# Optimization experiments

Measured on AMD Instinct MI355X. Metric: run time of the kernel, lower is better.

The kernel has to match this reference:

```python
import jax, jax.numpy as jnp
import numpy as np

BLOCK = 4  # block_size from init_kwargs


def space_to_channel_3d(x, b):
    # Faithful translation of SpaceToChannel_3d.forward (torch split/stack/permute chain).
    B, C, W, H, D = x.shape
    y = x.transpose(0, 2, 3, 4, 1)                      # (B, W, H, D, C)
    y = y.reshape(B, W, H, D // b, b, C)                # split depth into D//b chunks of b
    y = y.transpose(0, 3, 1, 2, 4, 5)                   # (B, D//b, W, H, b, C)
    y = y.reshape(B, D // b, W // b, H // b, C * b * b * b)  # per-chunk row-major reshape
    y = y.transpose(0, 2, 3, 1, 4)                      # (B, W//b, H//b, D//b, C*b^3)
    return y.transpose(0, 4, 1, 2, 3)                   # (B, C*b^3, W//b, H//b, D//b)


def channel_to_space_3d(x, b):
    # Faithful translation of ChannelToSpace_3d.forward.
    B, Cd, wd, hd, dd = x.shape
    b3 = b * b * b
    Cs = Cd // b3
    y = x.transpose(0, 2, 3, 4, 1)                      # (B, wd, hd, dd, Cd)
    y = y.reshape(B, wd, hd, dd, b * b, b, Cs)          # split b^3 dim into b^2 chunks of b
    y = y.transpose(0, 4, 1, 2, 3, 5, 6)                # (B, b^2, wd, hd, dd, b, Cs)
    y = y.reshape(B, b * b, wd, hd, dd * b, Cs)         # merge (dd, b) per chunk
    y = y.transpose(0, 2, 1, 3, 4, 5)                   # (B, wd, b^2, hd, dd*b, Cs)
    y = y.reshape(B, wd * b, hd * b, dd * b, Cs)        # row-major merge of (wd, b^2, hd)
    return y.transpose(0, 4, 1, 2, 3)                   # (B, Cs, wd*b, hd*b, dd*b)


def setup_inputs() -> dict:
    key = jax.random.key(0)
    k1, k2 = jax.random.split(key)
    x = jax.random.normal(k1, (4, 32, 64, 64, 64), dtype=jnp.float32)
    gamma = jax.random.normal(k2, (1,), dtype=jnp.float32)
    return {"x": x, "gamma": gamma}


def reference(x, gamma):
    b = BLOCK
    y = space_to_channel_3d(x, b)                       # (B, C*b^3, w, h, d)
    B, C, w, h, d = y.shape
    q = y.reshape(B, C, w * h * d)                      # (B, C', N)
    # channel-wise attention: energy (B, C', C')
    energy = jnp.einsum('bcn,ben->bce', q, q)
    energy_new = jnp.max(energy, axis=-1, keepdims=True) - energy
    attention = jax.nn.softmax(energy_new, axis=-1)
    out = jnp.einsum('bce,ben->bcn', attention, q)      # (B, C', N)
    out = out.reshape(B, C, w, h, d)
    out = gamma * out + y
    return channel_to_space_3d(out, b)
```

## Files before the change

### kernel.cpp

```cpp
#include <hip/hip_runtime.h>

typedef _Float16 f16;
typedef __attribute__((ext_vector_type(8))) _Float16 f16x8;
typedef __attribute__((ext_vector_type(4))) float f32x4;

#define CCH 2048
#define NSP 4096
#define NB  4

#define VMCNT8 asm volatile("s_waitcnt vmcnt(8)" ::: "memory")
#define VMCNT4 asm volatile("s_waitcnt vmcnt(4)" ::: "memory")
#define VMCNT0 asm volatile("s_waitcnt vmcnt(0)" ::: "memory")
#define CFENCE asm volatile("" ::: "memory")

__device__ __forceinline__ void gld16(const void* g, void* l) {
  __builtin_amdgcn_global_load_lds(
      (const __attribute__((address_space(1))) void*)g,
      (__attribute__((address_space(3))) void*)l, 16, 0, 0);
}

__global__ void pack_kernel(const float* __restrict__ x, f16* __restrict__ qh,
                            f16* __restrict__ qv, int b0) {
  int gid = blockIdx.x * 256 + threadIdx.x;
  int n = gid & (NSP - 1);
  int t = gid >> 12;
  int c = t & 31; t >>= 5;
  int r = t & 15; int ib = t >> 4;
  int wc = n >> 8, hc = (n >> 4) & 15, dc = n & 15;
  int w = wc * 4 + (hc >> 2);
  int h = (hc & 3) * 16 + r;
  int b = b0 + ib;
  const f32x4 v = *(const f32x4*)(x + ((((size_t)b * 32 + c) * 64 + w) * 64 + h) * 64 + dc * 4);
#pragma unroll
  for (int bd = 0; bd < 4; ++bd) {
    int cc = r * 128 + bd * 32 + c;
    size_t o = ((size_t)ib * CCH + cc) * NSP + n;
    float val = v[bd];
    f16 hi = (f16)val;
    qh[o] = hi;
    qv[o] = (f16)(2.0f * val - (float)hi);
  }
}

__global__ void transpose_kernel(const f16* __restrict__ qh, f16* __restrict__ qhT) {
  int ib = blockIdx.z;
  int j0 = blockIdx.x * 64, n0 = blockIdx.y * 64;
  __shared__ f16 tile[64][72];
  int t = threadIdx.x;
  int r = t >> 3;
  int cb = (t & 7) * 8;
#pragma unroll
  for (int half = 0; half < 2; ++half) {
    int rr = r + half * 32;
    f16x8 v = *(const f16x8*)(qh + ((size_t)ib * CCH + j0 + rr) * NSP + n0 + cb);
    *(f16x8*)&tile[rr][cb] = v;
  }
  __syncthreads();
#pragma unroll
  for (int half = 0; half < 2; ++half) {
    int rr = r + half * 32;
    f16x8 o;
#pragma unroll
    for (int u = 0; u < 8; ++u) o[u] = tile[cb + u][rr];
    *(f16x8*)(qhT + ((size_t)ib * NSP + n0 + rr) * CCH + j0 + cb) = o;
  }
}

__global__ __launch_bounds__(256) void gemm1_kernel(const f16* __restrict__ qh,
                                                    const f16* __restrict__ qv,
                                                    float* __restrict__ energy) {
  int ib = blockIdx.z;
  int bx = blockIdx.x;
  int tri = (bx & 7) * 17 + (bx >> 3);
  int rem = tri, bi = 0, span = 16;
  while (rem >= span) { rem -= span; ++bi; --span; }
  int bj = bi + rem;
  int i0 = bi * 128, j0 = bj * 128;
  float* eout = energy + (size_t)ib * CCH * CCH;

  __shared__ f16 Lds[2][4][128 * 32];
  int tid = threadIdx.x;
  int lane = tid & 63, wv = tid >> 6;
  int l15 = lane & 15, quad = lane >> 4;
  int wr = (wv >> 1) * 64, wcol = (wv & 1) * 64;
  int swz = (l15 >> 1) & 3;
  int kbs = (lane & 3) ^ ((lane >> 3) & 3);

  const f16* srcA = (wv & 1) ? qv : qh;
  int rbase = (wv < 2) ? i0 : j0;
  const f16* gsrc = srcA + ((size_t)ib * CCH + rbase) * NSP
                    + (size_t)(lane >> 2) * NSP + kbs * 8;

  auto stage = [&](int buf, int kk) {
    f16* ld = &Lds[buf][wv][0];
#pragma unroll
    for (int t = 0; t < 8; ++t)
      gld16(gsrc + (size_t)(t * 16) * NSP + kk, ld + t * 512);
  };

  const f32x4 vzero = {0.f, 0.f, 0.f, 0.f};
  f32x4 acc[4][4];
#pragma unroll
  for (int a = 0; a < 4; ++a)
#pragma unroll
    for (int bq = 0; bq < 4; ++bq) acc[a][bq] = vzero;

  const int nk = NSP >> 5;
  stage(0, 0);
  __syncthreads();
  for (int it = 0; it < nk; ++it) {
    int cur = it & 1;
    if (it + 1 < nk) stage(cur ^ 1, (it + 1) << 5);
    f16x8 ah[4], av[4], bh[4], bv[4];
#pragma unroll
    for (int mt = 0; mt < 4; ++mt) {
      int row = wr + mt * 16 + l15;
      ah[mt] = *(const f16x8*)&Lds[cur][0][row * 32 + ((quad ^ swz) * 8)];
      av[mt] = *(const f16x8*)&Lds[cur][1][row * 32 + ((quad ^ swz) * 8)];
    }
#pragma unroll
    for (int nt = 0; nt < 4; ++nt) {
      int col = wcol + nt * 16 + l15;
      bh[nt] = *(const f16x8*)&Lds[cur][2][col * 32 + ((quad ^ swz) * 8)];
      bv[nt] = *(const f16x8*)&Lds[cur][3][col * 32 + ((quad ^ swz) * 8)];
    }
    __builtin_amdgcn_s_setprio(1);
#pragma unroll
    for (int mt = 0; mt < 4; ++mt)
#pragma unroll
      for (int nt = 0; nt < 4; ++nt) {
        acc[mt][nt] = __builtin_amdgcn_mfma_f32_16x16x32_f16(ah[mt], bv[nt], acc[mt][nt], 0, 0, 0);
        acc[mt][nt] = __builtin_amdgcn_mfma_f32_16x16x32_f16(av[mt], bh[nt], acc[mt][nt], 0, 0, 0);
      }
    __builtin_amdgcn_s_setprio(0);
    __syncthreads();
  }
  bool diag = (bi == bj);
#pragma unroll
  for (int mt = 0; mt < 4; ++mt)
#pragma unroll
    for (int nt = 0; nt < 4; ++nt)
#pragma unroll
      for (int rg = 0; rg < 4; ++rg) {
        int row = i0 + wr + mt * 16 + quad * 4 + rg;
        int col = j0 + wcol + nt * 16 + l15;
        float v = 0.5f * acc[mt][nt][rg];
        eout[(size_t)row * CCH + col] = v;
        if (!diag) eout[(size_t)col * CCH + row] = v;
      }
}

__global__ void softmax_kernel(const float* __restrict__ e0,
                               const float* __restrict__ gamma_p,
                               f16* __restrict__ attn) {
  int i = blockIdx.x, ib = blockIdx.y;
  const float* r0 = e0 + ((size_t)ib * CCH + i) * CCH;
  f16* arow = attn + ((size_t)ib * CCH + i) * CCH;
  int t = threadIdx.x;
  f32x4 v0 = *(const f32x4*)(r0 + t * 8);
  f32x4 v1 = *(const f32x4*)(r0 + t * 8 + 4);
  float m = v0[0];
#pragma unroll
  for (int u = 1; u < 4; ++u) m = fminf(m, v0[u]);
#pragma unroll
  for (int u = 0; u < 4; ++u) m = fminf(m, v1[u]);
#pragma unroll
  for (int off = 32; off > 0; off >>= 1) m = fminf(m, __shfl_xor(m, off));
  __shared__ float redA[4], redB[4];
  if ((t & 63) == 0) redA[t >> 6] = m;
  __syncthreads();
  m = fminf(fminf(redA[0], redA[1]), fminf(redA[2], redA[3]));
  float e[8], s = 0.f;
#pragma unroll
  for (int u = 0; u < 4; ++u) { e[u] = __expf(m - v0[u]); s += e[u]; }
#pragma unroll
  for (int u = 0; u < 4; ++u) { e[4 + u] = __expf(m - v1[u]); s += e[4 + u]; }
#pragma unroll
  for (int off = 32; off > 0; off >>= 1) s += __shfl_xor(s, off);
  if ((t & 63) == 0) redB[t >> 6] = s;
  __syncthreads();
  s = redB[0] + redB[1] + redB[2] + redB[3];
  float gamma = *gamma_p;
  float ginv = gamma / s;
  int du = i - t * 8;
  f16x8 o;
#pragma unroll
  for (int u = 0; u < 8; ++u) {
    float v = e[u] * ginv;
    if (u == du) v += 1.0f;
    o[u] = (f16)v;
  }
  *(f16x8*)(arow + t * 8) = o;
}

__global__ __launch_bounds__(256) void gemm2_kernel(const f16* __restrict__ attn,
                                                    const f16* __restrict__ qhT,
                                                    float* __restrict__ out, int b0) {
  int ib = blockIdx.z;
  int lin = blockIdx.x + gridDim.x * blockIdx.y;
  int nwg = gridDim.x * gridDim.y;
  int cpx = nwg >> 3;
  int lin2 = (lin & 7) * cpx + (lin >> 3);
  int i0 = (lin2 & 15) * 128;
  int n0 = (lin2 >> 4) * 128;
  __shared__ f16 Lds[4][2][128 * 32];
  int tid = threadIdx.x;
  int lane = tid & 63, wv = tid >> 6;
  int l15 = lane & 15, quad = lane >> 4;
  int wr = (wv >> 1) * 64, wcol = (wv & 1) * 64;
  int swz = (l15 >> 1) & 3;
  int kbs = (lane & 3) ^ ((lane >> 3) & 3);

  int arr = wv >> 1, rh = wv & 1;
  const f16* gbase = arr ? (qhT + ((size_t)ib * NSP + n0) * CCH)
                         : (attn + ((size_t)ib * CCH + i0) * CCH);
  const f16* gsrc = gbase + (size_t)(rh * 64 + (lane >> 2)) * CCH + kbs * 8;

  auto stage = [&](int slot, int kk) {
#pragma unroll
    for (int t = 0; t < 4; ++t)
      gld16(gsrc + (size_t)(t * 16) * CCH + kk,
            &Lds[slot][arr][(rh * 64 + t * 16) * 32]);
  };

  const f32x4 vzero = {0.f, 0.f, 0.f, 0.f};
  f32x4 acc[4][4];
#pragma unroll
  for (int a = 0; a < 4; ++a)
#pragma unroll
    for (int bq = 0; bq < 4; ++bq) acc[a][bq] = vzero;

  const int NP = CCH / 32;
  stage(0, 0); stage(1, 32); stage(2, 64);
  for (int p = 0; p < NP; ++p) {
    int remp = NP - 1 - p;
    if (remp >= 2) { VMCNT8; } else if (remp == 1) { VMCNT4; } else { VMCNT0; }
    __builtin_amdgcn_s_barrier();
    CFENCE;
    if (p + 3 < NP) stage((p + 3) & 3, (p + 3) << 5);
    int s = p & 3;
    const f16* As = &Lds[s][0][0];
    const f16* Bs = &Lds[s][1][0];
    f16x8 af[4], bf[4];
#pragma unroll
    for (int mt = 0; mt < 4; ++mt)
      af[mt] = *(const f16x8*)&As[(wr + mt * 16 + l15) * 32 + ((quad ^ swz) * 8)];
#pragma unroll
    for (int nt = 0; nt < 4; ++nt)
      bf[nt] = *(const f16x8*)&Bs[(wcol + nt * 16 + l15) * 32 + ((quad ^ swz) * 8)];
    __builtin_amdgcn_s_setprio(1);
#pragma unroll
    for (int mt = 0; mt < 4; ++mt)
#pragma unroll
      for (int nt = 0; nt < 4; ++nt)
        acc[mt][nt] = __builtin_amdgcn_mfma_f32_16x16x32_f16(af[mt], bf[nt], acc[mt][nt], 0, 0, 0);
    __builtin_amdgcn_s_setprio(0);
  }

  __syncthreads();
  float* eld = (float*)&Lds[0][0][0];
#pragma unroll
  for (int mt = 0; mt < 4; ++mt) {
    int f = (wr >> 5) + (mt >> 1);
    int gb = (mt & 1) * 16 + quad * 4;
#pragma unroll
    for (int nt = 0; nt < 4; ++nt) {
      int jh = (wcol >> 4) + nt;
#pragma unroll
      for (int rg = 0; rg < 4; ++rg)
        eld[(gb + rg) * 512 + jh * 64 + l15 * 4 + f] = acc[mt][nt][rg];
    }
  }
  __syncthreads();
  int b = b0 + ib;
  int e = i0 >> 7;
  int iw = n0 >> 8;
  int W = iw * 4 + (e >> 2);
  int H0 = (e & 3) * 16 + ((n0 >> 4) & 15);
#pragma unroll
  for (int u = 0; u < 8; ++u) {
    int g = wv * 8 + u;
    size_t goff = ((((size_t)b * 32 + g) * 64 + W) * 4096) + (size_t)H0 * 64;
#pragma unroll
    for (int hv = 0; hv < 2; ++hv) {
      int fo = hv * 256 + lane * 4;
      *(f32x4*)(out + goff + fo) = *(const f32x4*)&eld[g * 512 + fo];
    }
  }
}

extern "C" void kernel_launch(void* const* d_in, const int* in_sizes, int n_in,
                              void* d_out, int out_size, void* d_ws, size_t ws_size,
                              hipStream_t stream) {
  const float* x = (const float*)d_in[0];
  const float* gamma = (const float*)d_in[1];
  float* out = (float*)d_out;

  const size_t szQ = (size_t)CCH * NSP;
  const size_t szE = (size_t)CCH * CCH;

  const size_t pb = szQ * 2 * 3 + szE * 4 + szE * 2;

  int nb = (ws_size >= (size_t)NB * pb) ? NB : 1;

  char* p = (char*)d_ws;
  f16* qh = (f16*)p;   p += (size_t)nb * szQ * 2;
  f16* qv = (f16*)p;   p += (size_t)nb * szQ * 2;
  f16* qhT = (f16*)p;  p += (size_t)nb * szQ * 2;
  float* energy = (float*)p; p += (size_t)nb * szE * 4;
  f16* attn = (f16*)p;

  for (int b0 = 0; b0 < NB; b0 += nb) {
    pack_kernel<<<nb * 8192, 256, 0, stream>>>(x, qh, qv, b0);
    transpose_kernel<<<dim3(32, 64, nb), 256, 0, stream>>>(qh, qhT);
    gemm1_kernel<<<dim3(136, 1, nb), 256, 0, stream>>>(qh, qv, energy);
    softmax_kernel<<<dim3(CCH, nb), 256, 0, stream>>>(energy, gamma, attn);
    gemm2_kernel<<<dim3(16, 32, nb), 256, 0, stream>>>(attn, qhT, out, b0);
  }
}
```

Measured before the change: 765.7 us.

## Use 3-term split-f16 energy GEMM and 256x256 tiles for output GEMM

The energy GEMM moves from a 2-MFMA symmetric trick (hi*v + v*hi, halved) to a 3-term hi*hi + hi*lo + lo*hi split, which adds one MFMA per tile step, likely for accuracy. The output GEMM moves to 512-thread workgroups with 256x256 tiles, a double buffer in place of the 4-slot vmcnt pipeline, and an epilogue staged through LDS in four passes. Larger tiles raise operand reuse but cut the pipeline depth and the number of workgroups, and gemm1 now does 50% more MFMA work.

```diff
diff --git a/kernel.cpp b/kernel.cpp
--- a/kernel.cpp
+++ b/kernel.cpp
@@ -7,11 +7,6 @@
 #define CCH 2048
 #define NSP 4096
 #define NB  4
-
-#define VMCNT8 asm volatile("s_waitcnt vmcnt(8)" ::: "memory")
-#define VMCNT4 asm volatile("s_waitcnt vmcnt(4)" ::: "memory")
-#define VMCNT0 asm volatile("s_waitcnt vmcnt(0)" ::: "memory")
-#define CFENCE asm volatile("" ::: "memory")
 
 __device__ __forceinline__ void gld16(const void* g, void* l) {
   __builtin_amdgcn_global_load_lds(
@@ -20,7 +15,7 @@
 }
 
 __global__ void pack_kernel(const float* __restrict__ x, f16* __restrict__ qh,
-                            f16* __restrict__ qv, int b0) {
+                            f16* __restrict__ ql, int b0) {
   int gid = blockIdx.x * 256 + threadIdx.x;
   int n = gid & (NSP - 1);
   int t = gid >> 12;
@@ -38,7 +33,7 @@
     float val = v[bd];
     f16 hi = (f16)val;
     qh[o] = hi;
-    qv[o] = (f16)(2.0f * val - (float)hi);
+    ql[o] = (f16)(val - (float)hi);
   }
 }
 
@@ -67,7 +62,7 @@
 }
 
 __global__ __launch_bounds__(256) void gemm1_kernel(const f16* __restrict__ qh,
-                                                    const f16* __restrict__ qv,
+                                                    const f16* __restrict__ ql,
                                                     float* __restrict__ energy) {
   int ib = blockIdx.z;
   int bx = blockIdx.x;
@@ -86,7 +81,7 @@
   int swz = (l15 >> 1) & 3;
   int kbs = (lane & 3) ^ ((lane >> 3) & 3);
 
-  const f16* srcA = (wv & 1) ? qv : qh;
+  const f16* srcA = (wv & 1) ? ql : qh;
   int rbase = (wv < 2) ? i0 : j0;
   const f16* gsrc = srcA + ((size_t)ib * CCH + rbase) * NSP
                     + (size_t)(lane >> 2) * NSP + kbs * 8;
@@ -111,26 +106,27 @@
   for (int it = 0; it < nk; ++it) {
     int cur = it & 1;
     if (it + 1 < nk) stage(cur ^ 1, (it + 1) << 5);
-    f16x8 ah[4], av[4], bh[4], bv[4];
+    f16x8 ah[4], al[4], bh[4], bl[4];
 #pragma unroll
     for (int mt = 0; mt < 4; ++mt) {
       int row = wr + mt * 16 + l15;
       ah[mt] = *(const f16x8*)&Lds[cur][0][row * 32 + ((quad ^ swz) * 8)];
-      av[mt] = *(const f16x8*)&Lds[cur][1][row * 32 + ((quad ^ swz) * 8)];
+      al[mt] = *(const f16x8*)&Lds[cur][1][row * 32 + ((quad ^ swz) * 8)];
     }
 #pragma unroll
     for (int nt = 0; nt < 4; ++nt) {
       int col = wcol + nt * 16 + l15;
       bh[nt] = *(const f16x8*)&Lds[cur][2][col * 32 + ((quad ^ swz) * 8)];
-      bv[nt] = *(const f16x8*)&Lds[cur][3][col * 32 + ((quad ^ swz) * 8)];
+      bl[nt] = *(const f16x8*)&Lds[cur][3][col * 32 + ((quad ^ swz) * 8)];
     }
     __builtin_amdgcn_s_setprio(1);
 #pragma unroll
     for (int mt = 0; mt < 4; ++mt)
 #pragma unroll
       for (int nt = 0; nt < 4; ++nt) {
-        acc[mt][nt] = __builtin_amdgcn_mfma_f32_16x16x32_f16(ah[mt], bv[nt], acc[mt][nt], 0, 0, 0);
-        acc[mt][nt] = __builtin_amdgcn_mfma_f32_16x16x32_f16(av[mt], bh[nt], acc[mt][nt], 0, 0, 0);
+        acc[mt][nt] = __builtin_amdgcn_mfma_f32_16x16x32_f16(ah[mt], bh[nt], acc[mt][nt], 0, 0, 0);
+        acc[mt][nt] = __builtin_amdgcn_mfma_f32_16x16x32_f16(ah[mt], bl[nt], acc[mt][nt], 0, 0, 0);
+        acc[mt][nt] = __builtin_amdgcn_mfma_f32_16x16x32_f16(al[mt], bh[nt], acc[mt][nt], 0, 0, 0);
       }
     __builtin_amdgcn_s_setprio(0);
     __syncthreads();
@@ -144,7 +140,7 @@
       for (int rg = 0; rg < 4; ++rg) {
         int row = i0 + wr + mt * 16 + quad * 4 + rg;
         int col = j0 + wcol + nt * 16 + l15;
-        float v = 0.5f * acc[mt][nt][rg];
+        float v = acc[mt][nt][rg];
         eout[(size_t)row * CCH + col] = v;
         if (!diag) eout[(size_t)col * CCH + row] = v;
       }
@@ -193,7 +189,7 @@
   *(f16x8*)(arow + t * 8) = o;
 }
 
-__global__ __launch_bounds__(256) void gemm2_kernel(const f16* __restrict__ attn,
+__global__ __launch_bounds__(512) void gemm2_kernel(const f16* __restrict__ attn,
                                                     const f16* __restrict__ qhT,
                                                     float* __restrict__ out, int b0) {
   int ib = blockIdx.z;
@@ -201,90 +197,92 @@
   int nwg = gridDim.x * gridDim.y;
   int cpx = nwg >> 3;
   int lin2 = (lin & 7) * cpx + (lin >> 3);
-  int i0 = (lin2 & 15) * 128;
-  int n0 = (lin2 >> 4) * 128;
-  __shared__ f16 Lds[4][2][128 * 32];
+  int i0 = (lin2 & 7) * 256;
+  int n0 = (lin2 >> 3) * 256;
+  __shared__ f16 Lds[2][2][256 * 32];
   int tid = threadIdx.x;
   int lane = tid & 63, wv = tid >> 6;
   int l15 = lane & 15, quad = lane >> 4;
-  int wr = (wv >> 1) * 64, wcol = (wv & 1) * 64;
+  int wr = (wv >> 2) * 128;
+  int wcol = (wv & 3) * 64;
   int swz = (l15 >> 1) & 3;
   int kbs = (lane & 3) ^ ((lane >> 3) & 3);
 
-  int arr = wv >> 1, rh = wv & 1;
+  int arr = wv >> 2, rsub = wv & 3;
   const f16* gbase = arr ? (qhT + ((size_t)ib * NSP + n0) * CCH)
                          : (attn + ((size_t)ib * CCH + i0) * CCH);
-  const f16* gsrc = gbase + (size_t)(rh * 64 + (lane >> 2)) * CCH + kbs * 8;
-
-  auto stage = [&](int slot, int kk) {
+  const f16* gsrc = gbase + (size_t)(rsub * 64 + (lane >> 2)) * CCH + kbs * 8;
+
+  auto stage = [&](int buf, int kk) {
 #pragma unroll
     for (int t = 0; t < 4; ++t)
       gld16(gsrc + (size_t)(t * 16) * CCH + kk,
-            &Lds[slot][arr][(rh * 64 + t * 16) * 32]);
+            &Lds[buf][arr][(rsub * 64 + t * 16) * 32]);
   };
 
   const f32x4 vzero = {0.f, 0.f, 0.f, 0.f};
-  f32x4 acc[4][4];
-#pragma unroll
-  for (int a = 0; a < 4; ++a)
+  f32x4 acc[8][4];
+#pragma unroll
+  for (int a = 0; a < 8; ++a)
 #pragma unroll
     for (int bq = 0; bq < 4; ++bq) acc[a][bq] = vzero;
 
-  const int NP = CCH / 32;
-  stage(0, 0); stage(1, 32); stage(2, 64);
-  for (int p = 0; p < NP; ++p) {
-    int remp = NP - 1 - p;
-    if (remp >= 2) { VMCNT8; } else if (remp == 1) { VMCNT4; } else { VMCNT0; }
-    __builtin_amdgcn_s_barrier();
-    CFENCE;
-    if (p + 3 < NP) stage((p + 3) & 3, (p + 3) << 5);
-    int s = p & 3;
-    const f16* As = &Lds[s][0][0];
-    const f16* Bs = &Lds[s][1][0];
-    f16x8 af[4], bf[4];
-#pragma unroll
-    for (int mt = 0; mt < 4; ++mt)
-      af[mt] = *(const f16x8*)&As[(wr + mt * 16 + l15) * 32 + ((quad ^ swz) * 8)];
+  const int nk = CCH >> 5;
+  stage(0, 0);
+  __syncthreads();
+  for (int it = 0; it < nk; ++it) {
+    int cur = it & 1;
+    if (it + 1 < nk) stage(cur ^ 1, (it + 1) << 5);
+    f16x8 af[8], bf[4];
+#pragma unroll
+    for (int mt = 0; mt < 8; ++mt)
+      af[mt] = *(const f16x8*)&Lds[cur][0][(wr + mt * 16 + l15) * 32 + ((quad ^ swz) * 8)];
 #pragma unroll
     for (int nt = 0; nt < 4; ++nt)
-      bf[nt] = *(const f16x8*)&Bs[(wcol + nt * 16 + l15) * 32 + ((quad ^ swz) * 8)];
+      bf[nt] = *(const f16x8*)&Lds[cur][1][(wcol + nt * 16 + l15) * 32 + ((quad ^ swz) * 8)];
     __builtin_amdgcn_s_setprio(1);
 #pragma unroll
-    for (int mt = 0; mt < 4; ++mt)
+    for (int mt = 0; mt < 8; ++mt)
 #pragma unroll
       for (int nt = 0; nt < 4; ++nt)
         acc[mt][nt] = __builtin_amdgcn_mfma_f32_16x16x32_f16(af[mt], bf[nt], acc[mt][nt], 0, 0, 0);
     __builtin_amdgcn_s_setprio(0);
-  }
-
-  __syncthreads();
+    __syncthreads();
+  }
+
   float* eld = (float*)&Lds[0][0][0];
-#pragma unroll
-  for (int mt = 0; mt < 4; ++mt) {
-    int f = (wr >> 5) + (mt >> 1);
-    int gb = (mt & 1) * 16 + quad * 4;
-#pragma unroll
-    for (int nt = 0; nt < 4; ++nt) {
-      int jh = (wcol >> 4) + nt;
-#pragma unroll
-      for (int rg = 0; rg < 4; ++rg)
-        eld[(gb + rg) * 512 + jh * 64 + l15 * 4 + f] = acc[mt][nt][rg];
+  int b = b0 + ib;
+#pragma unroll
+  for (int p = 0; p < 4; ++p) {
+    __syncthreads();
+    if ((wv >> 1) == p) {
+#pragma unroll
+      for (int mt = 0; mt < 8; ++mt) {
+        int f = mt >> 1;
+        int gb2 = (mt & 1) * 16 + quad * 4;
+#pragma unroll
+        for (int nt = 0; nt < 4; ++nt) {
+          int jh = (wv & 1) * 4 + nt;
+#pragma unroll
+          for (int rg = 0; rg < 4; ++rg)
+            eld[(gb2 + rg) * 512 + jh * 64 + l15 * 4 + f] = acc[mt][nt][rg];
+        }
+      }
     }
-  }
-  __syncthreads();
-  int b = b0 + ib;
-  int e = i0 >> 7;
-  int iw = n0 >> 8;
-  int W = iw * 4 + (e >> 2);
-  int H0 = (e & 3) * 16 + ((n0 >> 4) & 15);
-#pragma unroll
-  for (int u = 0; u < 8; ++u) {
-    int g = wv * 8 + u;
-    size_t goff = ((((size_t)b * 32 + g) * 64 + W) * 4096) + (size_t)H0 * 64;
-#pragma unroll
-    for (int hv = 0; hv < 2; ++hv) {
-      int fo = hv * 256 + lane * 4;
-      *(f32x4*)(out + goff + fo) = *(const f32x4*)&eld[g * 512 + fo];
+    __syncthreads();
+    int h = p >> 1, nh = p & 1;
+    int e = (i0 >> 7) + h;
+    int W = (n0 >> 8) * 4 + (e >> 2);
+    int H0 = (e & 3) * 16 + nh * 8;
+#pragma unroll
+    for (int u = 0; u < 4; ++u) {
+      int g = wv * 4 + u;
+      size_t goff = ((((size_t)b * 32 + g) * 64 + W) * 4096) + (size_t)H0 * 64;
+#pragma unroll
+      for (int hv = 0; hv < 2; ++hv) {
+        int fo = hv * 256 + lane * 4;
+        *(f32x4*)(out + goff + fo) = *(const f32x4*)&eld[g * 512 + fo];
+      }
     }
   }
 }
@@ -305,16 +303,16 @@
 
   char* p = (char*)d_ws;
   f16* qh = (f16*)p;   p += (size_t)nb * szQ * 2;
-  f16* qv = (f16*)p;   p += (size_t)nb * szQ * 2;
+  f16* ql = (f16*)p;   p += (size_t)nb * szQ * 2;
   f16* qhT = (f16*)p;  p += (size_t)nb * szQ * 2;
   float* energy = (float*)p; p += (size_t)nb * szE * 4;
   f16* attn = (f16*)p;
 
   for (int b0 = 0; b0 < NB; b0 += nb) {
-    pack_kernel<<<nb * 8192, 256, 0, stream>>>(x, qh, qv, b0);
+    pack_kernel<<<nb * 8192, 256, 0, stream>>>(x, qh, ql, b0);
     transpose_kernel<<<dim3(32, 64, nb), 256, 0, stream>>>(qh, qhT);
-    gemm1_kernel<<<dim3(136, 1, nb), 256, 0, stream>>>(qh, qv, energy);
+    gemm1_kernel<<<dim3(136, 1, nb), 256, 0, stream>>>(qh, ql, energy);
     softmax_kernel<<<dim3(CCH, nb), 256, 0, stream>>>(energy, gamma, attn);
-    gemm2_kernel<<<dim3(16, 32, nb), 256, 0, stream>>>(attn, qhT, out, b0);
-  }
-}
+    gemm2_kernel<<<dim3(8, 16, nb), 512, 0, stream>>>(attn, qhT, out, b0);
+  }
+}
```

After: 749.0 us. -2.2%, faster.
